# Kernel optimization log

Hardware: AMD Instinct MI355X
Metric: run time of the kernel (lower is better)

Reference implementation:

```python
import jax, jax.numpy as jnp
import numpy as np

EMBED_DIM = 384
B, P, N = 8, 4, 4096


def setup_inputs() -> dict:
    key = jax.random.key(0)
    k1, k2, k3, k4, k5 = jax.random.split(key, 5)
    scale = 1.0 / np.sqrt(EMBED_DIM)
    return {
        "x": jax.random.normal(k1, (B, EMBED_DIM, P, N), dtype=jnp.float32),
        "w_qkv": jax.random.normal(k2, (1 + 2 * EMBED_DIM, EMBED_DIM), dtype=jnp.float32) * scale,
        "b_qkv": jax.random.normal(k3, (1 + 2 * EMBED_DIM,), dtype=jnp.float32) * 0.01,
        "w_out": jax.random.normal(k4, (EMBED_DIM, EMBED_DIM), dtype=jnp.float32) * scale,
        "b_out": jax.random.normal(k5, (EMBED_DIM,), dtype=jnp.float32) * 0.01,
    }


def reference(x, w_qkv, b_qkv, w_out, b_out):
    # x: [B, C, P, N] (C=embed_dim, P=patch area, N=num patches)
    C = x.shape[1]
    # 1x1 conv qkv projection -> [B, 1+2C, P, N]
    qkv = jnp.einsum("bcpn,oc->bopn", x, w_qkv) + b_qkv[None, :, None, None]
    q = qkv[:, :1]            # [B, 1, P, N]
    k = qkv[:, 1:1 + C]       # [B, C, P, N]
    v = qkv[:, 1 + C:]        # [B, C, P, N]
    # softmax over spatial dim N (attn_dropout=0 -> identity)
    context_scores = jax.nn.softmax(q, axis=-1)
    # context vector: weighted sum over N -> [B, C, P, 1]
    context_vector = jnp.sum(k * context_scores, axis=-1, keepdims=True)
    # broadcast-multiply with relu(v)
    out = jax.nn.relu(v) * context_vector
    # 1x1 conv output projection
    out = jnp.einsum("bcpn,oc->bopn", out, w_out) + b_out[None, :, None, None]
    return out
```

## Files before the change

### kernel.cpp

```cpp
#include <hip/hip_runtime.h>
#include <hip/hip_bf16.h>
#include <stdint.h>

#define CC   384
#define BB   8
#define PP   4
#define NNN  4096
#define NBP  32
#define PN   (PP*NNN)

#define AS1 __attribute__((address_space(1)))
#define AS3 __attribute__((address_space(3)))

typedef float  f32x4 __attribute__((ext_vector_type(4)));
typedef short  s16x8 __attribute__((ext_vector_type(8)));
typedef unsigned short u16x4 __attribute__((ext_vector_type(4)));

__device__ __forceinline__ unsigned short f2bf(float f) {
  unsigned int u = __float_as_uint(f);
  u += 0x7fffu + ((u >> 16) & 1u);
  return (unsigned short)(u >> 16);
}
__device__ __forceinline__ float bf2f(unsigned short u) {
  return __uint_as_float(((unsigned int)u) << 16);
}

__device__ __forceinline__ int swz16(int r) {
  return ((r ^ (r >> 2)) & 15) << 4;
}

__device__ __forceinline__ void stage16(const char* g, char* l_uniform, int lane) {
#if defined(__has_builtin) && __has_builtin(__builtin_amdgcn_global_load_lds)
  __builtin_amdgcn_global_load_lds((const AS1 unsigned int*)g,
                                   (AS3 unsigned int*)l_uniform, 16, 0, 0);
#else
  *(int4*)(l_uniform + lane*16) = *(const int4*)g;
#endif
}


__global__ __launch_bounds__(256) void k_pre(
    const float* __restrict__ x, const float* __restrict__ wqkv,
    unsigned short* __restrict__ xbf, float* __restrict__ q)
{
  __shared__ __align__(16) unsigned short tr[24576];
  __shared__ float4 qw[64];
  char* trb = (char*)tr;
  const int bid = blockIdx.x;
  const int bp = bid >> 6, nt = bid & 63;
  const int b = bp >> 2, p = bp & 3;
  const int n0 = nt * 64;
  const int t  = threadIdx.x;
  const int wv_ = t >> 6, lane = t & 63;
  const int cg = t >> 4, nv = t & 15;
  const int r0 = 4 * nv;
  const float* xb = x + (size_t)b*CC*PN + (size_t)p*NNN + n0 + r0;
  const int s0 = swz16(r0+0), s1 = swz16(r0+1), s2 = swz16(r0+2), s3 = swz16(r0+3);

  float4 qa = {0.f, 0.f, 0.f, 0.f};
  #pragma unroll 3
  for (int it = 0; it < 12; ++it) {
    const int c0 = 32*it + 2*cg;
    const float4 x0 = *(const float4*)(xb + (size_t)c0*PN);
    const float4 x1 = *(const float4*)(xb + (size_t)(c0+1)*PN);
    const float w0 = wqkv[c0], w1 = wqkv[c0+1];
    qa.x += w0*x0.x + w1*x1.x;
    qa.y += w0*x0.y + w1*x1.y;
    qa.z += w0*x0.z + w1*x1.z;
    qa.w += w0*x0.w + w1*x1.w;
    const unsigned int p0 = (unsigned)f2bf(x0.x) | ((unsigned)f2bf(x1.x) << 16);
    const unsigned int p1 = (unsigned)f2bf(x0.y) | ((unsigned)f2bf(x1.y) << 16);
    const unsigned int p2 = (unsigned)f2bf(x0.z) | ((unsigned)f2bf(x1.z) << 16);
    const unsigned int p3 = (unsigned)f2bf(x0.w) | ((unsigned)f2bf(x1.w) << 16);
    const int cb = 2*c0;
    *(unsigned int*)(trb + (((r0+0)*768 + cb) ^ s0)) = p0;
    *(unsigned int*)(trb + (((r0+1)*768 + cb) ^ s1)) = p1;
    *(unsigned int*)(trb + (((r0+2)*768 + cb) ^ s2)) = p2;
    *(unsigned int*)(trb + (((r0+3)*768 + cb) ^ s3)) = p3;
  }
  qa.x += __shfl_xor(qa.x, 16); qa.y += __shfl_xor(qa.y, 16);
  qa.z += __shfl_xor(qa.z, 16); qa.w += __shfl_xor(qa.w, 16);
  qa.x += __shfl_xor(qa.x, 32); qa.y += __shfl_xor(qa.y, 32);
  qa.z += __shfl_xor(qa.z, 32); qa.w += __shfl_xor(qa.w, 32);
  if (lane < 16) qw[wv_*16 + lane] = qa;
  __syncthreads();
  const int4* trs = (const int4*)tr;
  int4* dst = (int4*)(xbf + (size_t)bid * 24576);
  #pragma unroll
  for (int j = 0; j < 12; ++j) dst[j*256 + t] = trs[j*256 + t];
  if (t < 16) {
    float4 a0 = qw[t], a1 = qw[16+t], a2 = qw[32+t], a3 = qw[48+t];
    float4 o; o.x = a0.x+a1.x+a2.x+a3.x; o.y = a0.y+a1.y+a2.y+a3.y;
    o.z = a0.z+a1.z+a2.z+a3.z; o.w = a0.w+a1.w+a2.w+a3.w;
    *(float4*)(q + (size_t)bp*NNN + n0 + 4*t) = o;
  }
}

__global__ __launch_bounds__(256) void k_wcvt2(
    const float* __restrict__ wqkv, const float* __restrict__ wout,
    unsigned short* __restrict__ wvt, unsigned short* __restrict__ woutt)
{
  const int i = blockIdx.x*256 + threadIdx.x;
  const int e = (i < CC*CC) ? i : i - CC*CC;
  const int j   = e & 7;
  const int g   = (e >> 3) & 3;
  const int l15 = (e >> 5) & 15;
  const int rem = e >> 9;
  const int ks  = rem % 12;
  const int mf  = rem / 12;
  const int row = 16*mf + l15;
  const int col = 32*ks + 8*g + j;
  if (i < CC*CC) wvt[e]          = f2bf(wqkv[(size_t)(385 + row)*CC + col]);
  else           woutt[e]        = f2bf(wout[(size_t)row*CC + col]);
}

__global__ __launch_bounds__(256) void k_softmax2(
    const float* __restrict__ q, const float* __restrict__ bqkv,
    float* __restrict__ scores)
{
  __shared__ float red[8];
  const int bp = blockIdx.x;
  const int t  = threadIdx.x;
  const int wv_ = t >> 6, ln = t & 63;
  const float bq = bqkv[0];
  float4 qv[4];
  float lmax = -1e30f;
  #pragma unroll
  for (int i = 0; i < 4; ++i) {
    const int n = i*1024 + t*4;
    float4 a = *(const float4*)(q + (size_t)bp*NNN + n);
    qv[i].x = a.x + bq; qv[i].y = a.y + bq; qv[i].z = a.z + bq; qv[i].w = a.w + bq;
    lmax = fmaxf(lmax, fmaxf(fmaxf(qv[i].x, qv[i].y), fmaxf(qv[i].z, qv[i].w)));
  }
  #pragma unroll
  for (int off = 32; off; off >>= 1) lmax = fmaxf(lmax, __shfl_xor(lmax, off));
  if (ln == 0) red[wv_] = lmax;
  __syncthreads();
  const float M = fmaxf(fmaxf(red[0], red[1]), fmaxf(red[2], red[3]));
  float lsum = 0.f;
  #pragma unroll
  for (int i = 0; i < 4; ++i) {
    qv[i].x = expf(qv[i].x - M); qv[i].y = expf(qv[i].y - M);
    qv[i].z = expf(qv[i].z - M); qv[i].w = expf(qv[i].w - M);
    lsum += qv[i].x + qv[i].y + qv[i].z + qv[i].w;
  }
  #pragma unroll
  for (int off = 32; off; off >>= 1) lsum += __shfl_xor(lsum, off);
  if (ln == 0) red[4 + wv_] = lsum;
  __syncthreads();
  const float inv = 1.f / (red[4] + red[5] + red[6] + red[7]);
  #pragma unroll
  for (int i = 0; i < 4; ++i) {
    const int n = i*1024 + t*4;
    float4 o; o.x=qv[i].x*inv; o.y=qv[i].y*inv; o.z=qv[i].z*inv; o.w=qv[i].w*inv;
    *(float4*)(scores + (size_t)bp*NNN + n) = o;
  }
}

__global__ __launch_bounds__(384) void k_xs2(
    const unsigned short* __restrict__ xbf, const float* __restrict__ scores,
    float* __restrict__ partial)
{
  __shared__ __align__(16) char lds[49152];
  __shared__ float sl[64];
  const int bid = blockIdx.x;
  const int bp = bid >> 6, nt = bid & 63;
  const int t = threadIdx.x;
  const int w6 = t >> 6, lane = t & 63;
  const char* gsrc = (const char*)xbf + (size_t)bid * 49152;
  #pragma unroll
  for (int r = 0; r < 8; ++r) {
    const int loff = (r*6 + w6) * 1024;
    stage16(gsrc + loff + lane*16, lds + loff, lane);
  }
  if (t < 64) sl[t] = scores[(size_t)bp*NNN + nt*64 + t];
  __syncthreads();
  float acc = 0.f;
  #pragma unroll 8
  for (int r = 0; r < 64; ++r) {
    const unsigned short uv = *(const unsigned short*)(lds + ((r*768 + 2*t) ^ swz16(r)));
    acc += bf2f(uv) * sl[r];
  }
  partial[(size_t)bid*CC + t] = acc;
}

__global__ __launch_bounds__(384) void k_cv2(
    const float* __restrict__ partial, const float* __restrict__ wqkv,
    const float* __restrict__ bqkv, float* __restrict__ cv)
{
  __shared__ float xsl[CC];
  const int bp = blockIdx.x;
  const int t  = threadIdx.x;
  float s = 0.f;
  #pragma unroll 8
  for (int nt = 0; nt < 64; ++nt) s += partial[((size_t)bp*64 + nt)*CC + t];
  xsl[t] = s;
  __syncthreads();
  float acc = bqkv[1 + t];
  const float* wk = wqkv + (size_t)(1 + t)*CC;
  #pragma unroll 8
  for (int c2 = 0; c2 < CC; ++c2) acc += wk[c2] * xsl[c2];
  cv[(size_t)bp*CC + t] = acc;
}

__device__ __forceinline__ void gemm_t(
    const unsigned short* __restrict__ wt, const char* lds,
    int w, int g, int l15, f32x4 acc[3][4])
{
  const unsigned short* base = wt + (size_t)(3*w)*12*512 + l15*32 + g*8;
  s16x8 a[3][3];
  #pragma unroll
  for (int pf = 0; pf < 3; ++pf)
    #pragma unroll
    for (int mi = 0; mi < 3; ++mi)
      a[pf][mi] = *(const s16x8*)(base + ((size_t)mi*12 + pf)*512);
  #pragma unroll
  for (int ks = 0; ks < 12; ++ks) {
    const int slot = ks % 3;
    s16x8 bfr[4];
    #pragma unroll
    for (int nt = 0; nt < 4; ++nt) {
      const int row = 16*nt + l15;
      const int byteb = (row*768 + 64*ks + 16*g) ^ swz16(row);
      bfr[nt] = *(const s16x8*)(lds + byteb);
    }
    #pragma unroll
    for (int mi = 0; mi < 3; ++mi)
      #pragma unroll
      for (int nt = 0; nt < 4; ++nt)
        acc[mi][nt] = __builtin_amdgcn_mfma_f32_16x16x32_bf16(
            a[slot][mi], bfr[nt], acc[mi][nt], 0, 0, 0);
    if (ks + 3 < 12) {
      #pragma unroll
      for (int mi = 0; mi < 3; ++mi)
        a[slot][mi] = *(const s16x8*)(base + ((size_t)mi*12 + ks + 3)*512);
    }
  }
}

__global__ __launch_bounds__(512, 4) void k_main2(
    const unsigned short* __restrict__ xbf,
    const unsigned short* __restrict__ wvt,
    const unsigned short* __restrict__ woutt,
    const float* __restrict__ cv,
    const float* __restrict__ bqkv,
    const float* __restrict__ bout,
    float* __restrict__ out)
{
  __shared__ __align__(16) char lds[49152];
  const int bid = blockIdx.x;
  const int nb  = bid & 63;
  const int bp  = bid >> 6;
  const int b = bp >> 2, p = bp & 3;
  const int n0 = nb * 64;
  const int tid  = threadIdx.x;
  const int w    = tid >> 6;
  const int lane = tid & 63;
  const int g    = lane >> 4;
  const int l15  = lane & 15;

  {
    const char* gsrc = (const char*)xbf + (size_t)bid * 49152;
    #pragma unroll
    for (int r = 0; r < 6; ++r) {
      const int loff = (r*8 + w) * 1024;
      stage16(gsrc + loff + lane*16, lds + loff, lane);
    }
  }
  __syncthreads();

  f32x4 acc[3][4];
  #pragma unroll
  for (int i = 0; i < 3; ++i)
    #pragma unroll
    for (int j = 0; j < 4; ++j) acc[i][j] = (f32x4){0.f,0.f,0.f,0.f};

  gemm_t(wvt, lds, w, g, l15, acc);
  __syncthreads();

  const float* cvp = cv + (size_t)bp*CC;
  #pragma unroll
  for (int mi = 0; mi < 3; ++mi) {
    const int m0 = 48*w + 16*mi + 4*g;
    const float* bv = bqkv + 385 + m0;
    const float b0 = bv[0], b1 = bv[1], b2 = bv[2], b3 = bv[3];
    const float4 cvv = *(const float4*)(cvp + m0);
    #pragma unroll
    for (int nt = 0; nt < 4; ++nt) {
      const int row = 16*nt + l15;
      const f32x4 t = acc[mi][nt];
      u16x4 pk = { f2bf(fmaxf(t[0]+b0, 0.f)*cvv.x), f2bf(fmaxf(t[1]+b1, 0.f)*cvv.y),
                   f2bf(fmaxf(t[2]+b2, 0.f)*cvv.z), f2bf(fmaxf(t[3]+b3, 0.f)*cvv.w) };
      const int byte0 = (row*768 + 2*m0) ^ swz16(row);
      *(u16x4*)(lds + byte0) = pk;
    }
  }
  __syncthreads();

  #pragma unroll
  for (int i = 0; i < 3; ++i)
    #pragma unroll
    for (int j = 0; j < 4; ++j) acc[i][j] = (f32x4){0.f,0.f,0.f,0.f};

  gemm_t(woutt, lds, w, g, l15, acc);

  float* fl = (float*)lds;
  float* outb = out + (size_t)b*CC*PN + (size_t)p*NNN + n0;
  #pragma unroll
  for (int half = 0; half < 2; ++half) {
    __syncthreads();
    #pragma unroll
    for (int mi = 0; mi < 3; ++mi) {
      const int m0 = 48*w + 16*mi + 4*g;
      const float4 bo = *(const float4*)(bout + m0);
      const int cswz = g << 3;
      #pragma unroll
      for (int nt2 = 0; nt2 < 2; ++nt2) {
        const f32x4 t = acc[mi][2*half + nt2];
        const int colh = (16*nt2 + l15) ^ cswz;
        fl[(m0+0)*32 + colh] = t[0] + bo.x;
        fl[(m0+1)*32 + colh] = t[1] + bo.y;
        fl[(m0+2)*32 + colh] = t[2] + bo.z;
        fl[(m0+3)*32 + colh] = t[3] + bo.w;
      }
    }
    __syncthreads();
    #pragma unroll
    for (int ps = 0; ps < 6; ++ps) {
      const int idx = ps*512 + tid;
      const int row = idx >> 3;
      const int nq  = idx & 7;
      const int qb  = (nq*4) ^ (((row >> 2) & 3) << 3);
      const f32x4 v = *(const f32x4*)(fl + row*32 + qb);
      __builtin_nontemporal_store(v, (f32x4*)(outb + (size_t)row*PN + 32*half + nq*4));
    }
  }
}


__global__ __launch_bounds__(256) void k_qpart(
    const float* __restrict__ x, const float* __restrict__ wqkv,
    float* __restrict__ qpart)
{
  const int bid = blockIdx.x;
  const int seg = bid & 3;
  const int nc  = (bid >> 2) & 3;
  const int bp  = bid >> 4;
  const int b = bp >> 2, p = bp & 3;
  const int n = nc * 1024 + threadIdx.x * 4;
  const float* xb = x + (size_t)b*CC*PN + (size_t)p*NNN + n;
  float ax = 0.f, ay = 0.f, az = 0.f, aw = 0.f;
  const int c0 = seg * 96;
  #pragma unroll 8
  for (int c = c0; c < c0 + 96; ++c) {
    const float w = wqkv[c];
    const float4 xv = *(const float4*)(xb + (size_t)c*PN);
    ax += w*xv.x; ay += w*xv.y; az += w*xv.z; aw += w*xv.w;
  }
  float4 o; o.x=ax; o.y=ay; o.z=az; o.w=aw;
  *(float4*)(qpart + (size_t)(seg*NBP + bp)*NNN + n) = o;
}

__global__ __launch_bounds__(256) void k_softmax(
    const float* __restrict__ qpart, const float* __restrict__ bqkv,
    float* __restrict__ scores)
{
  __shared__ float red[8];
  const int bp = blockIdx.x;
  const int t  = threadIdx.x;
  const int wv_ = t >> 6, ln = t & 63;
  const float bq = bqkv[0];
  float4 q[4];
  float lmax = -1e30f;
  #pragma unroll
  for (int i = 0; i < 4; ++i) {
    const int n = i*1024 + t*4;
    const float* base = qpart + (size_t)bp*NNN + n;
    const float4 a = *(const float4*)(base);
    const float4 b1 = *(const float4*)(base + (size_t)NBP*NNN);
    const float4 c1 = *(const float4*)(base + (size_t)2*NBP*NNN);
    const float4 d1 = *(const float4*)(base + (size_t)3*NBP*NNN);
    q[i].x = a.x+b1.x+c1.x+d1.x + bq;
    q[i].y = a.y+b1.y+c1.y+d1.y + bq;
    q[i].z = a.z+b1.z+c1.z+d1.z + bq;
    q[i].w = a.w+b1.w+c1.w+d1.w + bq;
    lmax = fmaxf(lmax, fmaxf(fmaxf(q[i].x, q[i].y), fmaxf(q[i].z, q[i].w)));
  }
  #pragma unroll
  for (int off = 32; off; off >>= 1) lmax = fmaxf(lmax, __shfl_xor(lmax, off));
  if (ln == 0) red[wv_] = lmax;
  __syncthreads();
  const float M = fmaxf(fmaxf(red[0], red[1]), fmaxf(red[2], red[3]));
  float lsum = 0.f;
  #pragma unroll
  for (int i = 0; i < 4; ++i) {
    q[i].x = expf(q[i].x - M); q[i].y = expf(q[i].y - M);
    q[i].z = expf(q[i].z - M); q[i].w = expf(q[i].w - M);
    lsum += q[i].x + q[i].y + q[i].z + q[i].w;
  }
  #pragma unroll
  for (int off = 32; off; off >>= 1) lsum += __shfl_xor(lsum, off);
  if (ln == 0) red[4 + wv_] = lsum;
  __syncthreads();
  const float inv = 1.f / (red[4] + red[5] + red[6] + red[7]);
  #pragma unroll
  for (int i = 0; i < 4; ++i) {
    const int n = i*1024 + t*4;
    float4 o; o.x=q[i].x*inv; o.y=q[i].y*inv; o.z=q[i].z*inv; o.w=q[i].w*inv;
    *(float4*)(scores + (size_t)bp*NNN + n) = o;
  }
}

__global__ __launch_bounds__(256) void k_xs(
    const float* __restrict__ x, const float* __restrict__ scores,
    float* __restrict__ xs)
{
  __shared__ float red[4];
  const int c  = blockIdx.x;
  const int bp = blockIdx.y;
  const int b = bp >> 2, p = bp & 3;
  const float* xr = x + ((size_t)b*CC + c)*PN + (size_t)p*NNN;
  const float* sr = scores + (size_t)bp*NNN;
  float acc = 0.f;
  #pragma unroll
  for (int i = 0; i < 4; ++i) {
    const int n = i*1024 + threadIdx.x*4;
    const float4 xv = *(const float4*)(xr + n);
    const float4 sv = *(const float4*)(sr + n);
    acc += xv.x*sv.x + xv.y*sv.y + xv.z*sv.z + xv.w*sv.w;
  }
  #pragma unroll
  for (int off = 32; off; off >>= 1) acc += __shfl_xor(acc, off);
  if ((threadIdx.x & 63) == 0) red[threadIdx.x >> 6] = acc;
  __syncthreads();
  if (threadIdx.x == 0) xs[(size_t)bp*CC + c] = red[0]+red[1]+red[2]+red[3];
}

__global__ __launch_bounds__(256) void k_wcvt(
    const float* __restrict__ wqkv, const float* __restrict__ wout,
    unsigned short* __restrict__ wv, unsigned short* __restrict__ woutb)
{
  const int i = blockIdx.x*256 + threadIdx.x;
  if (i < CC*CC) wv[i] = f2bf(wqkv[385*CC + i]);
  else           woutb[i - CC*CC] = f2bf(wout[i - CC*CC]);
}

__global__ __launch_bounds__(384) void k_cv(
    const float* __restrict__ wqkv, const float* __restrict__ bqkv,
    const float* __restrict__ xs, float* __restrict__ cv)
{
  __shared__ float xsl[CC];
  const int bp = blockIdx.x;
  const int t  = threadIdx.x;
  xsl[t] = xs[(size_t)bp*CC + t];
  __syncthreads();
  float acc = bqkv[1 + t];
  const float* wk = wqkv + (size_t)(1 + t)*CC;
  #pragma unroll 8
  for (int c2 = 0; c2 < CC; ++c2) acc += wk[c2] * xsl[c2];
  cv[(size_t)bp*CC + t] = acc;
}

__device__ __forceinline__ void stage_load(
    const float* __restrict__ xb, int w, int chunk, float s[12])
{
  const int c0 = 96*chunk + 12*w;
  const float* xc = xb + (size_t)c0 * PN;
  #pragma unroll
  for (int k = 0; k < 12; ++k) s[k] = xc[(size_t)k * PN];
}

__device__ __forceinline__ void stage_write(
    char* lds, int w, int n, int chunk, const float s[12])
{
  const int swz = (n & 15) << 4;
  const int c0 = 96*chunk + 12*w;
  #pragma unroll
  for (int j = 0; j < 3; ++j) {
    u16x4 pk = { f2bf(s[4*j]), f2bf(s[4*j+1]), f2bf(s[4*j+2]), f2bf(s[4*j+3]) };
    const int byte0 = (n*768 + 2*(c0 + 4*j)) ^ swz;
    *(u16x4*)(lds + byte0) = pk;
  }
}

template<int KSN>
__device__ __forceinline__ void gemm_ks(
    const unsigned short* __restrict__ wa, const char* lds,
    int w, int g, int l15, int ks0, f32x4 acc[3][4])
{
  const unsigned short* wb = wa + (size_t)(48*w + l15)*CC + 8*g;
  s16x8 afr[2][3];
  #pragma unroll
  for (int mi = 0; mi < 3; ++mi)
    afr[0][mi] = *(const s16x8*)(wb + (size_t)(16*mi)*CC + 32*ks0);
  #pragma unroll
  for (int i = 0; i < KSN; ++i) {
    const int ks  = ks0 + i;
    const int cur = i & 1;
    if (i + 1 < KSN) {
      #pragma unroll
      for (int mi = 0; mi < 3; ++mi)
        afr[cur ^ 1][mi] = *(const s16x8*)(wb + (size_t)(16*mi)*CC + 32*(ks+1));
    }
    s16x8 bfr[4];
    #pragma unroll
    for (int nt = 0; nt < 4; ++nt) {
      const int row = 16*nt + l15;
      const int byteb = (row*768 + 64*ks + 16*g) ^ (l15 << 4);
      bfr[nt] = *(const s16x8*)(lds + byteb);
    }
    #pragma unroll
    for (int mi = 0; mi < 3; ++mi)
      #pragma unroll
      for (int nt = 0; nt < 4; ++nt)
        acc[mi][nt] = __builtin_amdgcn_mfma_f32_16x16x32_bf16(
            afr[cur][mi], bfr[nt], acc[mi][nt], 0, 0, 0);
  }
}

__global__ __launch_bounds__(512, 4) void k_main(
    const float* __restrict__ x,
    const unsigned short* __restrict__ wv,
    const unsigned short* __restrict__ woutb,
    const float* __restrict__ cv,
    const float* __restrict__ bqkv,
    const float* __restrict__ bout,
    float* __restrict__ out)
{
  __shared__ __align__(16) unsigned short lds_u16[64*384];
  char* lds = (char*)lds_u16;
  const int bid = blockIdx.x;
  const int nb  = bid & 63;
  const int bp  = bid >> 6;
  const int b = bp >> 2, p = bp & 3;
  const int n0 = nb * 64;
  const int tid  = threadIdx.x;
  const int w    = tid >> 6;
  const int lane = tid & 63;
  const int g    = lane >> 4;
  const int l15  = lane & 15;

  const float* xb = x + (size_t)b*CC*PN + (size_t)p*NNN + n0 + lane;

  float s[12];
  stage_load(xb, w, 0, s);
  stage_write(lds, w, lane, 0, s);
  stage_load(xb, w, 1, s);
  __syncthreads();

  f32x4 acc[3][4];
  #pragma unroll
  for (int i = 0; i < 3; ++i)
    #pragma unroll
    for (int j = 0; j < 4; ++j) acc[i][j] = (f32x4){0.f,0.f,0.f,0.f};

  for (int c = 0; c < 4; ++c) {
    gemm_ks<3>(wv, lds, w, g, l15, 3*c, acc);
    if (c < 3) {
      stage_write(lds, w, lane, c+1, s);
      if (c < 2) stage_load(xb, w, c+2, s);
    }
    __syncthreads();
  }

  const float* cvp = cv + (size_t)bp*CC;
  #pragma unroll
  for (int mi = 0; mi < 3; ++mi) {
    const int m0 = 48*w + 16*mi + 4*g;
    const float* bv = bqkv + 385 + m0;
    const float b0 = bv[0], b1 = bv[1], b2 = bv[2], b3 = bv[3];
    const float4 cvv = *(const float4*)(cvp + m0);
    #pragma unroll
    for (int nt = 0; nt < 4; ++nt) {
      const int row = 16*nt + l15;
      const f32x4 t = acc[mi][nt];
      u16x4 pk = { f2bf(fmaxf(t[0]+b0, 0.f)*cvv.x), f2bf(fmaxf(t[1]+b1, 0.f)*cvv.y),
                   f2bf(fmaxf(t[2]+b2, 0.f)*cvv.z), f2bf(fmaxf(t[3]+b3, 0.f)*cvv.w) };
      const int byte0 = (row*768 + 2*m0) ^ (l15 << 4);
      *(u16x4*)(lds + byte0) = pk;
    }
  }
  __syncthreads();

  #pragma unroll
  for (int i = 0; i < 3; ++i)
    #pragma unroll
    for (int j = 0; j < 4; ++j) acc[i][j] = (f32x4){0.f,0.f,0.f,0.f};

  gemm_ks<12>(woutb, lds, w, g, l15, 0, acc);

  #pragma unroll
  for (int mi = 0; mi < 3; ++mi) {
    const int m0 = 48*w + 16*mi + 4*g;
    const float4 bo = *(const float4*)(bout + m0);
    #pragma unroll
    for (int nt = 0; nt < 4; ++nt) {
      const int nn = n0 + 16*nt + l15;
      const f32x4 t = acc[mi][nt];
      float* ob = out + ((size_t)b*CC + m0)*PN + (size_t)p*NNN + nn;
      ob[0]            = t[0] + bo.x;
      ob[(size_t)PN]   = t[1] + bo.y;
      ob[2*(size_t)PN] = t[2] + bo.z;
      ob[3*(size_t)PN] = t[3] + bo.w;
    }
  }
}

extern "C" void kernel_launch(void* const* d_in, const int* in_sizes, int n_in,
                              void* d_out, int out_size, void* d_ws, size_t ws_size,
                              hipStream_t stream) {
  const float* x    = (const float*)d_in[0];
  const float* wqkv = (const float*)d_in[1];
  const float* bqkv = (const float*)d_in[2];
  const float* wout = (const float*)d_in[3];
  const float* bout = (const float*)d_in[4];
  float* out = (float*)d_out;
  char* ws = (char*)d_ws;

  const size_t OFF_XBF = 0;
  const size_t OFF_Q   = 100663296;
  const size_t OFF_SC  = 101187584;
  const size_t OFF_PT  = 101711872;
  const size_t OFF_WVT = 104857600;
  const size_t OFF_WOT = 105152512;
  const size_t OFF_CV  = 105447424;
  const size_t NEED    = 105496576;

  if (ws_size >= NEED) {
    unsigned short* xbf   = (unsigned short*)(ws + OFF_XBF);
    float* q              = (float*)(ws + OFF_Q);
    float* scores         = (float*)(ws + OFF_SC);
    float* partial        = (float*)(ws + OFF_PT);
    unsigned short* wvt   = (unsigned short*)(ws + OFF_WVT);
    unsigned short* woutt = (unsigned short*)(ws + OFF_WOT);
    float* cvp            = (float*)(ws + OFF_CV);

    hipLaunchKernelGGL(k_pre,      dim3(2048), dim3(256), 0, stream, x, wqkv, xbf, q);
    hipLaunchKernelGGL(k_wcvt2,    dim3(1152), dim3(256), 0, stream, wqkv, wout, wvt, woutt);
    hipLaunchKernelGGL(k_softmax2, dim3(32),   dim3(256), 0, stream, q, bqkv, scores);
    hipLaunchKernelGGL(k_xs2,      dim3(2048), dim3(384), 0, stream, xbf, scores, partial);
    hipLaunchKernelGGL(k_cv2,      dim3(32),   dim3(384), 0, stream, partial, wqkv, bqkv, cvp);
    hipLaunchKernelGGL(k_main2,    dim3(2048), dim3(512), 0, stream, xbf, wvt, woutt, cvp, bqkv, bout, out);
  } else {
    float* scores         = (float*)(ws);
    float* qpart          = (float*)(ws + 524288);
    float* xs             = (float*)(ws + 2621440);
    unsigned short* wv    = (unsigned short*)(ws + 2719744);
    unsigned short* woutb = (unsigned short*)(ws + 3014656);
    float* cvp            = (float*)(ws + 3309568);

    hipLaunchKernelGGL(k_qpart,   dim3(512),      dim3(256), 0, stream, x, wqkv, qpart);
    hipLaunchKernelGGL(k_wcvt,    dim3(1152),     dim3(256), 0, stream, wqkv, wout, wv, woutb);
    hipLaunchKernelGGL(k_softmax, dim3(32),       dim3(256), 0, stream, qpart, bqkv, scores);
    hipLaunchKernelGGL(k_xs,      dim3(CC, NBP),  dim3(256), 0, stream, x, scores, xs);
    hipLaunchKernelGGL(k_cv,      dim3(NBP),      dim3(384), 0, stream, wqkv, bqkv, xs, cvp);
    hipLaunchKernelGGL(k_main,    dim3(2048),     dim3(512), 0, stream, x, wv, woutb, cvp, bqkv, bout, out);
  }
}
```

Measured before the change: 241.4 us.

## Widen main fused GEMM tile to 128 columns with 12 waves per block

```diff
diff --git a/kernel.cpp b/kernel.cpp
--- a/kernel.cpp
+++ b/kernel.cpp
@@ -203,42 +203,42 @@
   cv[(size_t)bp*CC + t] = acc;
 }
 
-__device__ __forceinline__ void gemm_t(
+__device__ __forceinline__ void gemm_t2(
     const unsigned short* __restrict__ wt, const char* lds,
-    int w, int g, int l15, f32x4 acc[3][4])
-{
-  const unsigned short* base = wt + (size_t)(3*w)*12*512 + l15*32 + g*8;
-  s16x8 a[3][3];
+    int w, int g, int l15, f32x4 acc[2][8])
+{
+  const unsigned short* base = wt + (size_t)(2*w)*12*512 + l15*32 + g*8;
+  s16x8 a[3][2];
   #pragma unroll
   for (int pf = 0; pf < 3; ++pf)
     #pragma unroll
-    for (int mi = 0; mi < 3; ++mi)
+    for (int mi = 0; mi < 2; ++mi)
       a[pf][mi] = *(const s16x8*)(base + ((size_t)mi*12 + pf)*512);
   #pragma unroll
   for (int ks = 0; ks < 12; ++ks) {
     const int slot = ks % 3;
-    s16x8 bfr[4];
-    #pragma unroll
-    for (int nt = 0; nt < 4; ++nt) {
-      const int row = 16*nt + l15;
-      const int byteb = (row*768 + 64*ks + 16*g) ^ swz16(row);
+    s16x8 bfr[8];
+    #pragma unroll
+    for (int nt = 0; nt < 8; ++nt) {
+      const int row = 16*(nt & 3) + l15;
+      const int byteb = (nt >> 2)*49152 + ((row*768 + 64*ks + 16*g) ^ swz16(row));
       bfr[nt] = *(const s16x8*)(lds + byteb);
     }
     #pragma unroll
-    for (int mi = 0; mi < 3; ++mi)
+    for (int mi = 0; mi < 2; ++mi)
       #pragma unroll
-      for (int nt = 0; nt < 4; ++nt)
+      for (int nt = 0; nt < 8; ++nt)
         acc[mi][nt] = __builtin_amdgcn_mfma_f32_16x16x32_bf16(
             a[slot][mi], bfr[nt], acc[mi][nt], 0, 0, 0);
     if (ks + 3 < 12) {
       #pragma unroll
-      for (int mi = 0; mi < 3; ++mi)
+      for (int mi = 0; mi < 2; ++mi)
         a[slot][mi] = *(const s16x8*)(base + ((size_t)mi*12 + ks + 3)*512);
     }
   }
 }
 
-__global__ __launch_bounds__(512, 4) void k_main2(
+__global__ __launch_bounds__(768, 1) void k_main2b(
     const unsigned short* __restrict__ xbf,
     const unsigned short* __restrict__ wvt,
     const unsigned short* __restrict__ woutt,
@@ -247,92 +247,90 @@
     const float* __restrict__ bout,
     float* __restrict__ out)
 {
-  __shared__ __align__(16) char lds[49152];
+  __shared__ __align__(16) char lds[98304];
   const int bid = blockIdx.x;
-  const int nb  = bid & 63;
-  const int bp  = bid >> 6;
+  const int bp  = bid >> 5;
+  const int t2  = bid & 31;
   const int b = bp >> 2, p = bp & 3;
-  const int n0 = nb * 64;
-  const int tid  = threadIdx.x;
-  const int w    = tid >> 6;
+  const int tid = threadIdx.x;
+  const int w = tid >> 6;
   const int lane = tid & 63;
-  const int g    = lane >> 4;
-  const int l15  = lane & 15;
+  const int g = lane >> 4, l15 = lane & 15;
 
   {
-    const char* gsrc = (const char*)xbf + (size_t)bid * 49152;
-    #pragma unroll
-    for (int r = 0; r < 6; ++r) {
-      const int loff = (r*8 + w) * 1024;
+    const char* gsrc = (const char*)xbf + (size_t)(bp*64 + t2*2) * 49152;
+    #pragma unroll
+    for (int r = 0; r < 8; ++r) {
+      const int loff = (r*12 + w) * 1024;
       stage16(gsrc + loff + lane*16, lds + loff, lane);
     }
   }
   __syncthreads();
 
-  f32x4 acc[3][4];
-  #pragma unroll
-  for (int i = 0; i < 3; ++i)
-    #pragma unroll
-    for (int j = 0; j < 4; ++j) acc[i][j] = (f32x4){0.f,0.f,0.f,0.f};
-
-  gemm_t(wvt, lds, w, g, l15, acc);
+  f32x4 acc[2][8];
+  #pragma unroll
+  for (int i = 0; i < 2; ++i)
+    #pragma unroll
+    for (int j = 0; j < 8; ++j) acc[i][j] = (f32x4){0.f,0.f,0.f,0.f};
+
+  gemm_t2(wvt, lds, w, g, l15, acc);
   __syncthreads();
 
   const float* cvp = cv + (size_t)bp*CC;
   #pragma unroll
-  for (int mi = 0; mi < 3; ++mi) {
-    const int m0 = 48*w + 16*mi + 4*g;
+  for (int mi = 0; mi < 2; ++mi) {
+    const int m0 = 32*w + 16*mi + 4*g;
     const float* bv = bqkv + 385 + m0;
     const float b0 = bv[0], b1 = bv[1], b2 = bv[2], b3 = bv[3];
     const float4 cvv = *(const float4*)(cvp + m0);
     #pragma unroll
-    for (int nt = 0; nt < 4; ++nt) {
-      const int row = 16*nt + l15;
+    for (int nt = 0; nt < 8; ++nt) {
+      const int row = 16*(nt & 3) + l15;
       const f32x4 t = acc[mi][nt];
       u16x4 pk = { f2bf(fmaxf(t[0]+b0, 0.f)*cvv.x), f2bf(fmaxf(t[1]+b1, 0.f)*cvv.y),
                    f2bf(fmaxf(t[2]+b2, 0.f)*cvv.z), f2bf(fmaxf(t[3]+b3, 0.f)*cvv.w) };
-      const int byte0 = (row*768 + 2*m0) ^ swz16(row);
+      const int byte0 = (nt >> 2)*49152 + ((row*768 + 2*m0) ^ swz16(row));
       *(u16x4*)(lds + byte0) = pk;
     }
   }
   __syncthreads();
 
   #pragma unroll
-  for (int i = 0; i < 3; ++i)
-    #pragma unroll
-    for (int j = 0; j < 4; ++j) acc[i][j] = (f32x4){0.f,0.f,0.f,0.f};
-
-  gemm_t(woutt, lds, w, g, l15, acc);
+  for (int i = 0; i < 2; ++i)
+    #pragma unroll
+    for (int j = 0; j < 8; ++j) acc[i][j] = (f32x4){0.f,0.f,0.f,0.f};
+
+  gemm_t2(woutt, lds, w, g, l15, acc);
 
   float* fl = (float*)lds;
-  float* outb = out + (size_t)b*CC*PN + (size_t)p*NNN + n0;
   #pragma unroll
   for (int half = 0; half < 2; ++half) {
     __syncthreads();
     #pragma unroll
-    for (int mi = 0; mi < 3; ++mi) {
-      const int m0 = 48*w + 16*mi + 4*g;
+    for (int mi = 0; mi < 2; ++mi) {
+      const int m0 = 32*w + 16*mi + 4*g;
       const float4 bo = *(const float4*)(bout + m0);
       const int cswz = g << 3;
       #pragma unroll
-      for (int nt2 = 0; nt2 < 2; ++nt2) {
-        const f32x4 t = acc[mi][2*half + nt2];
+      for (int nt2 = 0; nt2 < 4; ++nt2) {
+        const f32x4 t = acc[mi][4*half + nt2];
         const int colh = (16*nt2 + l15) ^ cswz;
-        fl[(m0+0)*32 + colh] = t[0] + bo.x;
-        fl[(m0+1)*32 + colh] = t[1] + bo.y;
-        fl[(m0+2)*32 + colh] = t[2] + bo.z;
-        fl[(m0+3)*32 + colh] = t[3] + bo.w;
+        fl[(m0+0)*64 + colh] = t[0] + bo.x;
+        fl[(m0+1)*64 + colh] = t[1] + bo.y;
+        fl[(m0+2)*64 + colh] = t[2] + bo.z;
+        fl[(m0+3)*64 + colh] = t[3] + bo.w;
       }
     }
     __syncthreads();
-    #pragma unroll
-    for (int ps = 0; ps < 6; ++ps) {
-      const int idx = ps*512 + tid;
-      const int row = idx >> 3;
-      const int nq  = idx & 7;
+    float* outb = out + (size_t)b*CC*PN + (size_t)p*NNN + t2*128 + half*64;
+    #pragma unroll
+    for (int ps = 0; ps < 8; ++ps) {
+      const int idx = ps*768 + tid;
+      const int row = idx >> 4;
+      const int nq  = idx & 15;
       const int qb  = (nq*4) ^ (((row >> 2) & 3) << 3);
-      const f32x4 v = *(const f32x4*)(fl + row*32 + qb);
-      __builtin_nontemporal_store(v, (f32x4*)(outb + (size_t)row*PN + 32*half + nq*4));
+      const f32x4 v = *(const f32x4*)(fl + row*64 + qb);
+      __builtin_nontemporal_store(v, (f32x4*)(outb + (size_t)row*PN + nq*4));
     }
   }
 }
@@ -640,7 +638,7 @@
     hipLaunchKernelGGL(k_softmax2, dim3(32),   dim3(256), 0, stream, q, bqkv, scores);
     hipLaunchKernelGGL(k_xs2,      dim3(2048), dim3(384), 0, stream, xbf, scores, partial);
     hipLaunchKernelGGL(k_cv2,      dim3(32),   dim3(384), 0, stream, partial, wqkv, bqkv, cvp);
-    hipLaunchKernelGGL(k_main2,    dim3(2048), dim3(512), 0, stream, xbf, wvt, woutt, cvp, bqkv, bout, out);
+    hipLaunchKernelGGL(k_main2b,   dim3(1024), dim3(768), 0, stream, xbf, wvt, woutt, cvp, bqkv, bout, out);
   } else {
     float* scores         = (float*)(ws);
     float* qpart          = (float*)(ws + 524288);
```

New measurement: 233.3 us. 3.4% less time.
